# Kernel optimization log

Hardware: AMD Instinct MI355X
Metric: run time of the kernel (lower is better)

The kernel has to match this reference:

```python
import jax, jax.numpy as jnp
import numpy as np

B, L, D = 4, 64, 64
REL_NUM = 16
EMB_NUM = 10000
NEG = -1e9


def gru(x, Wih, Whh, bih, bhh):
    # torch nn.GRU (batch_first), single layer, zero initial state.
    # x: (B,L,Din); Wih: (3H,Din); Whh: (3H,H)
    H = Whh.shape[1]
    gx = x @ Wih.T + bih  # (B,L,3H) precompute input projections

    def step(h, gxt):
        gh = h @ Whh.T + bhh
        xr, xz, xn = jnp.split(gxt, 3, axis=-1)
        hr, hz, hn = jnp.split(gh, 3, axis=-1)
        rg = jax.nn.sigmoid(xr + hr)
        zg = jax.nn.sigmoid(xz + hz)
        ng = jnp.tanh(xn + rg * hn)
        h_new = (1.0 - zg) * ng + zg * h
        return h_new, h_new

    h0 = jnp.zeros((x.shape[0], H), x.dtype)
    _, ys = jax.lax.scan(step, h0, jnp.swapaxes(gx, 0, 1))
    return jnp.swapaxes(ys, 0, 1)  # (B,L,H)


def setup_inputs() -> dict:
    key = jax.random.key(0)
    ks = jax.random.split(key, 20)
    D2 = D // 2
    emb_table = jax.random.normal(ks[0], (EMB_NUM + 1, D), jnp.float32) * 0.1
    emb_table = emb_table.at[0].set(0.0)  # padding_idx=0
    rel_table = jax.random.normal(ks[1], (REL_NUM, D * D), jnp.float32) * 0.05
    rel_table = rel_table.at[0].set(0.0)  # padding_idx=0
    inp = {
        "x": jax.random.randint(ks[2], (B, L), 0, EMB_NUM, jnp.int64) if False else jax.random.randint(ks[2], (B, L), 0, EMB_NUM).astype(jnp.int32),
        "y": jax.random.randint(ks[3], (B,), 0, 2).astype(jnp.int32),
        "r": jax.random.randint(ks[4], (B, L, L), 0, REL_NUM).astype(jnp.int32),
        "l": jax.random.randint(ks[5], (B,), 0, 63).astype(jnp.int32),
        "emb_table": emb_table,
        "rel_table": rel_table,
        "attn_out_W": jax.random.normal(ks[6], (D, D), jnp.float32) * 0.1,
        "attn_out_b": jnp.zeros((D,), jnp.float32),
        "gru_Wih": jax.random.normal(ks[7], (3 * D, D), jnp.float32) * 0.1,
        "gru_Whh": jax.random.normal(ks[8], (3 * D, D), jnp.float32) * 0.1,
        "gru_bih": jax.random.normal(ks[9], (3 * D,), jnp.float32) * 0.01,
        "gru_bhh": jax.random.normal(ks[10], (3 * D,), jnp.float32) * 0.01,
        "out_Wih": jax.random.normal(ks[11], (3, D), jnp.float32) * 0.1,
        "out_Whh": jax.random.normal(ks[12], (3, 1), jnp.float32) * 0.1,
        "out_bih": jax.random.normal(ks[13], (3,), jnp.float32) * 0.01,
        "out_bhh": jax.random.normal(ks[14], (3,), jnp.float32) * 0.01,
        "cls_W1": jax.random.normal(ks[15], (D2, D), jnp.float32) * 0.1,
        "cls_b1": jnp.zeros((D2,), jnp.float32),
        "cls_W2": jax.random.normal(ks[16], (2, D2), jnp.float32) * 0.1,
        "cls_b2": jnp.zeros((2,), jnp.float32),
    }
    return inp


def reference(x, y, r, l, emb_table, rel_table, attn_out_W, attn_out_b,
              gru_Wih, gru_Whh, gru_bih, gru_bhh,
              out_Wih, out_Whh, out_bih, out_bhh,
              cls_W1, cls_b1, cls_W2, cls_b2):
    o = emb_table[x]  # (B,L,D)

    # faithful to torch loop bug: mask[:, :l[i]+1]=1 for all i -> cols < max(l)+1
    mask = jnp.arange(L) < (jnp.max(l) + 1)  # (L,)

    # RelationAttentionBatch: gather per-(i,j) DxD relation matrix, two matvecs
    rel = rel_table[r].reshape(r.shape[0], L, L, D, D)  # (B,L,L,D,D) big gather
    scores = jnp.einsum('bid,bijde,bje->bij', o, rel, o)  # q^T M k
    scores = jnp.where(r > 0, scores, NEG)
    p_attn = jax.nn.softmax(scores, axis=-1)  # dropout off (eval)
    o = jnp.einsum('bij,bjd->bid', p_attn, o) @ attn_out_W.T + attn_out_b

    # GRU layer
    o = gru(o, gru_Wih, gru_Whh, gru_bih, gru_bhh)  # (B,L,D)

    # output GRU -> global attention pooling
    ga = gru(o, out_Wih, out_Whh, out_bih, out_bhh)[..., 0]  # (B,L)
    ga = jnp.where(mask[None, :], ga, NEG)
    ga = jax.nn.softmax(ga, axis=-1)
    c = jnp.einsum('bl,bld->bd', ga, o)  # (B,D)

    # classifier (dropout off)
    h = jax.nn.relu(c @ cls_W1.T + cls_b1)
    logits = h @ cls_W2.T + cls_b2  # (B,2)
    y_hat = jax.nn.softmax(logits, axis=-1)
    logp = jax.nn.log_softmax(logits, axis=-1)
    loss = -jnp.mean(logp[jnp.arange(logits.shape[0]), y])
    return y_hat, loss
```

## Files before the change

### kernel.cpp

```cpp
#include <hip/hip_runtime.h>
#include <math.h>

#define BB 4
#define LL 64
#define DD 64
#define NEG_ -1e9f
#define NBALLAST 480
#define LOG2E 1.44269504088896340736f

typedef _Float16 h2 __attribute__((ext_vector_type(2)));

__device__ __forceinline__ float rcp_(float x) { return __builtin_amdgcn_rcpf(x); }
__device__ __forceinline__ float fast_sigmoid(float x) { return rcp_(1.0f + __expf(-x)); }
__device__ __forceinline__ float fast_tanh(float x) { return fmaf(-2.0f, rcp_(__expf(2.0f * x) + 1.0f), 1.0f); }

__global__ __launch_bounds__(256) void attn_kernel(
    const int* __restrict__ x, const int* __restrict__ r,
    const float* __restrict__ emb, const float* __restrict__ rel,
    const float* __restrict__ aW, const float* __restrict__ ab,
    const float* __restrict__ Wih, const float* __restrict__ bih,
    float* __restrict__ gx, int* __restrict__ done)
{
    const int i = blockIdx.x, b = blockIdx.y;
    const int tt = threadIdx.x, lane = tt & 63, wv = tt >> 6;
    __shared__ float o_lds[LL][DD + 1];
    __shared__ float w_lds[16][DD + 1];
    __shared__ float p_lds[LL];
    __shared__ float pv_part[4][DD];
    __shared__ float ao_lds[DD];
    __shared__ float o2_lds[DD];

    if (i == 0 && b == 0 && tt == 0) *done = 0;

    {
        const int j = tt >> 2, q = tt & 3;
        const int row = x[b * LL + j];
        const float4* src = (const float4*)(emb + row * DD + q * 16);
        const float4 v0 = src[0], v1 = src[1], v2 = src[2], v3 = src[3];
        float* dst = &o_lds[j][q * 16];
        dst[0] = v0.x; dst[1] = v0.y; dst[2] = v0.z; dst[3] = v0.w;
        dst[4] = v1.x; dst[5] = v1.y; dst[6] = v1.z; dst[7] = v1.w;
        dst[8] = v2.x; dst[9] = v2.y; dst[10] = v2.z; dst[11] = v2.w;
        dst[12] = v3.x; dst[13] = v3.y; dst[14] = v3.z; dst[15] = v3.w;
    }
    __syncthreads();

    {
        const int eq = lane & 15, dq = lane >> 4;
#pragma unroll
        for (int kk = 0; kk < 4; kk++) {
            const int k = wv * 4 + kk + 1;
            if (k <= 15) {
                float4 acc = make_float4(0.f, 0.f, 0.f, 0.f);
                const float* relb = rel + k * 4096 + eq * 4;
#pragma unroll
                for (int g2 = 0; g2 < 16; g2++) {
                    const int d = g2 * 4 + dq;
                    const float od = o_lds[i][d];
                    const float4 rv4 = *(const float4*)(relb + d * 64);
                    acc.x = fmaf(od, rv4.x, acc.x);
                    acc.y = fmaf(od, rv4.y, acc.y);
                    acc.z = fmaf(od, rv4.z, acc.z);
                    acc.w = fmaf(od, rv4.w, acc.w);
                }
                acc.x += __shfl_xor(acc.x, 16, 64); acc.y += __shfl_xor(acc.y, 16, 64);
                acc.z += __shfl_xor(acc.z, 16, 64); acc.w += __shfl_xor(acc.w, 16, 64);
                acc.x += __shfl_xor(acc.x, 32, 64); acc.y += __shfl_xor(acc.y, 32, 64);
                acc.z += __shfl_xor(acc.z, 32, 64); acc.w += __shfl_xor(acc.w, 32, 64);
                if (dq == 0) {
                    float* wd = &w_lds[k][eq * 4];
                    wd[0] = acc.x; wd[1] = acc.y; wd[2] = acc.z; wd[3] = acc.w;
                }
            }
        }
    }
    __syncthreads();

    if (wv == 0) {
        const int rv = r[(b * LL + i) * LL + lane];
        float s = NEG_;
        if (rv > 0) {
            float a0 = 0.f, a1 = 0.f;
#pragma unroll
            for (int e = 0; e < DD; e += 2) {
                a0 = fmaf(w_lds[rv][e + 0], o_lds[lane][e + 0], a0);
                a1 = fmaf(w_lds[rv][e + 1], o_lds[lane][e + 1], a1);
            }
            s = a0 + a1;
        }
        float mx = s;
        for (int off = 1; off < 64; off <<= 1) mx = fmaxf(mx, __shfl_xor(mx, off, 64));
        const float ex = __expf(s - mx);
        float sum = ex;
        for (int off = 1; off < 64; off <<= 1) sum += __shfl_xor(sum, off, 64);
        p_lds[lane] = ex * rcp_(sum);
    }
    __syncthreads();

    {
        float acc = 0.f;
#pragma unroll
        for (int j = 0; j < 16; j++) {
            const int jj = wv * 16 + j;
            acc = fmaf(p_lds[jj], o_lds[jj][lane], acc);
        }
        pv_part[wv][lane] = acc;
    }
    __syncthreads();
    if (wv == 0)
        ao_lds[lane] = (pv_part[0][lane] + pv_part[1][lane]) + (pv_part[2][lane] + pv_part[3][lane]);
    __syncthreads();

    {
        const int row = tt >> 2, q = tt & 3;
        float a = 0.f;
        const float4* wr4 = (const float4*)(aW + row * DD + q * 16);
#pragma unroll
        for (int e4 = 0; e4 < 4; e4++) {
            const float4 w4 = wr4[e4];
            const float* av = &ao_lds[q * 16 + e4 * 4];
            a = fmaf(av[0], w4.x, a); a = fmaf(av[1], w4.y, a);
            a = fmaf(av[2], w4.z, a); a = fmaf(av[3], w4.w, a);
        }
        a += __shfl_xor(a, 1, 64);
        a += __shfl_xor(a, 2, 64);
        if (q == 0) o2_lds[row] = a + ab[row];
    }
    __syncthreads();

    if (tt < 192) {
        float a = bih[tt];
        const float4* wg4 = (const float4*)(Wih + tt * DD);
#pragma unroll 4
        for (int e4 = 0; e4 < 16; e4++) {
            const float4 w4 = wg4[e4];
            const float* ov = &o2_lds[e4 * 4];
            a = fmaf(ov[0], w4.x, a); a = fmaf(ov[1], w4.y, a);
            a = fmaf(ov[2], w4.z, a); a = fmaf(ov[3], w4.w, a);
        }
        const float scale = (tt < 128) ? -LOG2E : (2.0f * LOG2E);
        gx[(b * LL + i) * 192 + tt] = a * scale;
    }
}

__global__ __launch_bounds__(128, 1) void gru2_kernel(
    const float* __restrict__ gx, const float* __restrict__ Whh, const float* __restrict__ bhh,
    const float* __restrict__ oWih, const float* __restrict__ oWhh,
    const float* __restrict__ obih, const float* __restrict__ obhh,
    const int* __restrict__ lvec, float* __restrict__ cws, int* __restrict__ done,
    const int* __restrict__ y,
    const float* __restrict__ W1, const float* __restrict__ b1,
    const float* __restrict__ W2, const float* __restrict__ b2,
    float* __restrict__ bsink, float* __restrict__ out)
{
    const int tt = threadIdx.x, t = tt & 63, wv = tt >> 6;

    if (blockIdx.x >= BB) {
        float a0 = tt * 1e-6f, a1 = a0 + 1.f, a2 = a0 + 2.f, a3 = a0 + 3.f;
#pragma unroll 8
        for (int it = 0; it < 2000; it++) {
            a0 = fmaf(a0, 1.0000001f, 1e-7f);
            a1 = fmaf(a1, 1.0000001f, 1e-7f);
            a2 = fmaf(a2, 1.0000001f, 1e-7f);
            a3 = fmaf(a3, 1.0000001f, 1e-7f);
        }
        bsink[(blockIdx.x - BB) * 128 + tt] = (a0 + a1) + (a2 + a3);
        return;
    }

    const int b = blockIdx.x;
    __shared__ float gx_lds[LL][192];
    __shared__ float o3[LL][DD + 1];
    __shared__ int prog;
    __shared__ float c_lds[DD];
    __shared__ float h1s[32];
    __shared__ float lgs[2];

    {
        const float4* src = (const float4*)(gx + b * LL * 192);
        float4* dst = (float4*)&gx_lds[0][0];
#pragma unroll 4
        for (int f = 0; f < 24; f++) dst[f * 128 + tt] = src[f * 128 + tt];
    }
    if (tt == 0) prog = 0;
    __syncthreads();

    if (wv == 0) {
        h2 whr[32], whz[32], whn[32];
        {
            const float4* r0 = (const float4*)(Whh + t * DD);
            const float4* r1 = (const float4*)(Whh + (DD + t) * DD);
            const float4* r2 = (const float4*)(Whh + (2 * DD + t) * DD);
#pragma unroll
            for (int e = 0; e < 16; e++) {
                const float4 a = r0[e], bq = r1[e], c = r2[e];
                whr[2 * e + 0] = (h2){(_Float16)(-LOG2E * a.x), (_Float16)(-LOG2E * a.y)};
                whr[2 * e + 1] = (h2){(_Float16)(-LOG2E * a.z), (_Float16)(-LOG2E * a.w)};
                whz[2 * e + 0] = (h2){(_Float16)(-LOG2E * bq.x), (_Float16)(-LOG2E * bq.y)};
                whz[2 * e + 1] = (h2){(_Float16)(-LOG2E * bq.z), (_Float16)(-LOG2E * bq.w)};
                whn[2 * e + 0] = (h2){(_Float16)(2.f * LOG2E * c.x), (_Float16)(2.f * LOG2E * c.y)};
                whn[2 * e + 1] = (h2){(_Float16)(2.f * LOG2E * c.z), (_Float16)(2.f * LOG2E * c.w)};
            }
        }
#pragma unroll
        for (int i2 = 0; i2 < 32; i2++) {
            asm volatile("" : "+v"(whr[i2]), "+v"(whz[i2]), "+v"(whn[i2]));
        }
        const float br = -LOG2E * bhh[t];
        const float bz = -LOG2E * bhh[DD + t];
        const float bn = 2.f * LOG2E * bhh[2 * DD + t];

        float h = 0.0f;
        int pki = 0;
        float g_r = gx_lds[0][t], g_z = gx_lds[0][DD + t], g_n = gx_lds[0][2 * DD + t];

#pragma unroll 1
        for (int l = 0; l < LL; l++) {
            const int ln = (l + 1) & 63;
            const float pg_r = gx_lds[ln][t];
            const float pg_z = gx_lds[ln][DD + t];
            const float pg_n = gx_lds[ln][2 * DD + t];

            float ra0 = g_r + br, ra1 = 0.f, ra2 = 0.f, ra3 = 0.f;
            float za0 = g_z + bz, za1 = 0.f, za2 = 0.f, za3 = 0.f;
            float na0 = bn,       na1 = 0.f, na2 = 0.f, na3 = 0.f;
#pragma unroll
            for (int j = 0; j < 8; j++) {
                const h2 p0 = __builtin_bit_cast(h2, __builtin_amdgcn_readlane(pki, 8 * j + 0));
                const h2 p1 = __builtin_bit_cast(h2, __builtin_amdgcn_readlane(pki, 8 * j + 2));
                const h2 p2_ = __builtin_bit_cast(h2, __builtin_amdgcn_readlane(pki, 8 * j + 4));
                const h2 p3 = __builtin_bit_cast(h2, __builtin_amdgcn_readlane(pki, 8 * j + 6));
                ra0 = __builtin_amdgcn_fdot2(p0, whr[4 * j + 0], ra0, false);
                ra1 = __builtin_amdgcn_fdot2(p1, whr[4 * j + 1], ra1, false);
                ra2 = __builtin_amdgcn_fdot2(p2_, whr[4 * j + 2], ra2, false);
                ra3 = __builtin_amdgcn_fdot2(p3, whr[4 * j + 3], ra3, false);
                za0 = __builtin_amdgcn_fdot2(p0, whz[4 * j + 0], za0, false);
                za1 = __builtin_amdgcn_fdot2(p1, whz[4 * j + 1], za1, false);
                za2 = __builtin_amdgcn_fdot2(p2_, whz[4 * j + 2], za2, false);
                za3 = __builtin_amdgcn_fdot2(p3, whz[4 * j + 3], za3, false);
                na0 = __builtin_amdgcn_fdot2(p0, whn[4 * j + 0], na0, false);
                na1 = __builtin_amdgcn_fdot2(p1, whn[4 * j + 1], na1, false);
                na2 = __builtin_amdgcn_fdot2(p2_, whn[4 * j + 2], na2, false);
                na3 = __builtin_amdgcn_fdot2(p3, whn[4 * j + 3], na3, false);
            }
            const float yr = (ra0 + ra1) + (ra2 + ra3);
            const float yz = (za0 + za1) + (za2 + za3);
            const float hn = (na0 + na1) + (na2 + na3);

            const float rg = rcp_(1.0f + __builtin_amdgcn_exp2f(yr));
            const float zg = rcp_(1.0f + __builtin_amdgcn_exp2f(yz));
            const float ng = fmaf(-2.0f,
                rcp_(1.0f + __builtin_amdgcn_exp2f(fmaf(rg, hn, g_n))), 1.0f);
            h = fmaf(zg, h - ng, ng);
            o3[l][t] = h;

            if ((l & 3) == 3 && t == 0)
                __hip_atomic_store(&prog, l + 1, __ATOMIC_RELEASE,
                                   __HIP_MEMORY_SCOPE_WORKGROUP);

            const int hxi = __builtin_amdgcn_update_dpp(
                0, __builtin_bit_cast(int, h), 0xB1, 0xF, 0xF, true);
            pki = __builtin_bit_cast(int,
                __builtin_amdgcn_cvt_pkrtz(h, __builtin_bit_cast(float, hxi)));

            g_r = pg_r; g_z = pg_z; g_n = pg_n;
        }
        return;
    }

    const float wm0 = oWih[t], wm1 = oWih[DD + t], wm2 = oWih[2 * DD + t];
    const float ob0 = obih[0], ob1 = obih[1], ob2 = obih[2];
    const float w0 = oWhh[0], w1 = oWhh[1], w2 = oWhh[2];
    const float c0 = obhh[0], c1 = obhh[1], c2 = obhh[2];
    const int maxl = max(max(lvec[0], lvec[1]), max(lvec[2], lvec[3]));

    float hh = 0.0f, pv = 0.0f;
#pragma unroll 1
    for (int l = 0; l < LL; l++) {
        if ((l & 3) == 0) {
            while (__hip_atomic_load(&prog, __ATOMIC_ACQUIRE,
                                     __HIP_MEMORY_SCOPE_WORKGROUP) < l + 1) {}
        }
        const float o = o3[l][t];
        float s0 = o * wm0, s1 = o * wm1, s2 = o * wm2;
#pragma unroll
        for (int off = 1; off < 64; off <<= 1) {
            s0 += __shfl_xor(s0, off, 64);
            s1 += __shfl_xor(s1, off, 64);
            s2 += __shfl_xor(s2, off, 64);
        }
        const float rg = fast_sigmoid(s0 + ob0 + fmaf(hh, w0, c0));
        const float zg = fast_sigmoid(s1 + ob1 + fmaf(hh, w1, c1));
        const float ng = fast_tanh(s2 + ob2 + rg * fmaf(hh, w2, c2));
        hh = (1.0f - zg) * ng + zg * hh;
        pv = (t == l) ? hh : pv;
    }

    {
        const float v = (t <= maxl) ? pv : NEG_;
        float mx = v;
        for (int off = 1; off < 64; off <<= 1) mx = fmaxf(mx, __shfl_xor(mx, off, 64));
        const float ex = __expf(v - mx);
        float sum = ex;
        for (int off = 1; off < 64; off <<= 1) sum += __shfl_xor(sum, off, 64);
        pv = ex * rcp_(sum);
    }

    {
        float acc = 0.f;
#pragma unroll 8
        for (int l = 0; l < LL; l++) {
            const float p = __shfl(pv, l, 64);
            acc = fmaf(p, o3[l][t], acc);
        }
        __hip_atomic_store(&cws[b * DD + t], acc, __ATOMIC_RELAXED,
                           __HIP_MEMORY_SCOPE_AGENT);
    }
    __threadfence();
    unsigned int old = 0;
    if (t == 0)
        old = __hip_atomic_fetch_add((unsigned int*)done, 1u, __ATOMIC_ACQ_REL,
                                     __HIP_MEMORY_SCOPE_AGENT);
    old = __shfl(old, 0, 64);

    if (old == BB - 1) {
        __threadfence();
        float loss = 0.0f;
        for (int bb = 0; bb < BB; bb++) {
            c_lds[t] = __hip_atomic_load(&cws[bb * DD + t], __ATOMIC_RELAXED,
                                         __HIP_MEMORY_SCOPE_AGENT);
            if (t < 32) {
                float a = b1[t];
                const float* wr = W1 + t * DD;
                for (int d = 0; d < DD; d++) a = fmaf(c_lds[d], wr[d], a);
                h1s[t] = fmaxf(a, 0.0f);
            }
            if (t < 2) {
                float a = b2[t];
                const float* wr = W2 + t * 32;
                for (int m2 = 0; m2 < 32; m2++) a = fmaf(h1s[m2], wr[m2], a);
                lgs[t] = a;
            }
            if (t == 0) {
                const float l0 = lgs[0], l1 = lgs[1];
                const float mx = fmaxf(l0, l1);
                const float e0 = __expf(l0 - mx), e1 = __expf(l1 - mx);
                const float s = e0 + e1;
                out[bb * 2 + 0] = e0 / s;
                out[bb * 2 + 1] = e1 / s;
                const float lp = ((y[bb] == 1) ? l1 : l0) - mx - __logf(s);
                loss -= lp * 0.25f;
            }
        }
        if (t == 0) out[8] = loss;
    }
}

extern "C" void kernel_launch(void* const* d_in, const int* in_sizes, int n_in,
                              void* d_out, int out_size, void* d_ws, size_t ws_size,
                              hipStream_t stream)
{
    const int*   x    = (const int*)d_in[0];
    const int*   y    = (const int*)d_in[1];
    const int*   r    = (const int*)d_in[2];
    const int*   l    = (const int*)d_in[3];
    const float* emb  = (const float*)d_in[4];
    const float* rel  = (const float*)d_in[5];
    const float* aW   = (const float*)d_in[6];
    const float* ab   = (const float*)d_in[7];
    const float* Wih  = (const float*)d_in[8];
    const float* Whh  = (const float*)d_in[9];
    const float* bih  = (const float*)d_in[10];
    const float* bhh  = (const float*)d_in[11];
    const float* oWih = (const float*)d_in[12];
    const float* oWhh = (const float*)d_in[13];
    const float* obih = (const float*)d_in[14];
    const float* obhh = (const float*)d_in[15];
    const float* W1   = (const float*)d_in[16];
    const float* b1   = (const float*)d_in[17];
    const float* W2   = (const float*)d_in[18];
    const float* b2   = (const float*)d_in[19];

    float* ws    = (float*)d_ws;
    float* gx    = ws;
    float* cws   = ws + 49152;
    int*   done  = (int*)(ws + 49152 + 256);
    float* bsink = ws + 49152 + 256 + 64;

    attn_kernel<<<dim3(LL, BB), 256, 0, stream>>>(x, r, emb, rel, aW, ab, Wih, bih,
                                                  gx, done);
    gru2_kernel<<<BB + NBALLAST, 128, 0, stream>>>(gx, Whh, bhh, oWih, oWhh, obih,
                                                   obhh, l, cws, done, y, W1, b1,
                                                   W2, b2, bsink, (float*)d_out);
}
```

Before: 46.47 us.

## Fuse attention and GRU kernels into one launch with per-row readiness flags

Merges the attention kernel and the GRU/pooling kernel into a single launch. The extra blocks per batch run the GRU and spin on per-row flags published by the attention blocks, so the recurrence can start on early rows while later rows are still being computed. The GRU now reads gx from global memory one step ahead instead of staging it all in LDS, and the busy-work ballast blocks are removed. The cost is a memset launch to clear the flags, and a deadlock risk if the attention blocks cannot all be resident at once.

```diff
diff --git a/kernel.cpp b/kernel.cpp
--- a/kernel.cpp
+++ b/kernel.cpp
@@ -5,7 +5,6 @@
 #define LL 64
 #define DD 64
 #define NEG_ -1e9f
-#define NBALLAST 480
 #define LOG2E 1.44269504088896340736f
 
 typedef _Float16 h2 __attribute__((ext_vector_type(2)));
@@ -14,178 +13,182 @@
 __device__ __forceinline__ float fast_sigmoid(float x) { return rcp_(1.0f + __expf(-x)); }
 __device__ __forceinline__ float fast_tanh(float x) { return fmaf(-2.0f, rcp_(__expf(2.0f * x) + 1.0f), 1.0f); }
 
-__global__ __launch_bounds__(256) void attn_kernel(
+struct AttnS {
+    float o_lds[LL][DD + 1];
+    float w_lds[16][DD + 1];
+    float p_lds[LL];
+    float pv_part[4][DD];
+    float ao_lds[DD];
+    float o2_lds[DD];
+};
+struct GruS {
+    float o3[LL][DD + 1];
+    float c_lds[DD];
+    float h1s[32];
+    float lgs[2];
+};
+
+__global__ __launch_bounds__(256, 1) void mega_kernel(
     const int* __restrict__ x, const int* __restrict__ r,
     const float* __restrict__ emb, const float* __restrict__ rel,
     const float* __restrict__ aW, const float* __restrict__ ab,
     const float* __restrict__ Wih, const float* __restrict__ bih,
-    float* __restrict__ gx, int* __restrict__ done)
-{
-    const int i = blockIdx.x, b = blockIdx.y;
-    const int tt = threadIdx.x, lane = tt & 63, wv = tt >> 6;
-    __shared__ float o_lds[LL][DD + 1];
-    __shared__ float w_lds[16][DD + 1];
-    __shared__ float p_lds[LL];
-    __shared__ float pv_part[4][DD];
-    __shared__ float ao_lds[DD];
-    __shared__ float o2_lds[DD];
-
-    if (i == 0 && b == 0 && tt == 0) *done = 0;
-
-    {
-        const int j = tt >> 2, q = tt & 3;
-        const int row = x[b * LL + j];
-        const float4* src = (const float4*)(emb + row * DD + q * 16);
-        const float4 v0 = src[0], v1 = src[1], v2 = src[2], v3 = src[3];
-        float* dst = &o_lds[j][q * 16];
-        dst[0] = v0.x; dst[1] = v0.y; dst[2] = v0.z; dst[3] = v0.w;
-        dst[4] = v1.x; dst[5] = v1.y; dst[6] = v1.z; dst[7] = v1.w;
-        dst[8] = v2.x; dst[9] = v2.y; dst[10] = v2.z; dst[11] = v2.w;
-        dst[12] = v3.x; dst[13] = v3.y; dst[14] = v3.z; dst[15] = v3.w;
-    }
-    __syncthreads();
-
-    {
-        const int eq = lane & 15, dq = lane >> 4;
-#pragma unroll
-        for (int kk = 0; kk < 4; kk++) {
-            const int k = wv * 4 + kk + 1;
-            if (k <= 15) {
-                float4 acc = make_float4(0.f, 0.f, 0.f, 0.f);
-                const float* relb = rel + k * 4096 + eq * 4;
-#pragma unroll
-                for (int g2 = 0; g2 < 16; g2++) {
-                    const int d = g2 * 4 + dq;
-                    const float od = o_lds[i][d];
-                    const float4 rv4 = *(const float4*)(relb + d * 64);
-                    acc.x = fmaf(od, rv4.x, acc.x);
-                    acc.y = fmaf(od, rv4.y, acc.y);
-                    acc.z = fmaf(od, rv4.z, acc.z);
-                    acc.w = fmaf(od, rv4.w, acc.w);
-                }
-                acc.x += __shfl_xor(acc.x, 16, 64); acc.y += __shfl_xor(acc.y, 16, 64);
-                acc.z += __shfl_xor(acc.z, 16, 64); acc.w += __shfl_xor(acc.w, 16, 64);
-                acc.x += __shfl_xor(acc.x, 32, 64); acc.y += __shfl_xor(acc.y, 32, 64);
-                acc.z += __shfl_xor(acc.z, 32, 64); acc.w += __shfl_xor(acc.w, 32, 64);
-                if (dq == 0) {
-                    float* wd = &w_lds[k][eq * 4];
-                    wd[0] = acc.x; wd[1] = acc.y; wd[2] = acc.z; wd[3] = acc.w;
-                }
-            }
-        }
-    }
-    __syncthreads();
-
-    if (wv == 0) {
-        const int rv = r[(b * LL + i) * LL + lane];
-        float s = NEG_;
-        if (rv > 0) {
-            float a0 = 0.f, a1 = 0.f;
-#pragma unroll
-            for (int e = 0; e < DD; e += 2) {
-                a0 = fmaf(w_lds[rv][e + 0], o_lds[lane][e + 0], a0);
-                a1 = fmaf(w_lds[rv][e + 1], o_lds[lane][e + 1], a1);
-            }
-            s = a0 + a1;
-        }
-        float mx = s;
-        for (int off = 1; off < 64; off <<= 1) mx = fmaxf(mx, __shfl_xor(mx, off, 64));
-        const float ex = __expf(s - mx);
-        float sum = ex;
-        for (int off = 1; off < 64; off <<= 1) sum += __shfl_xor(sum, off, 64);
-        p_lds[lane] = ex * rcp_(sum);
-    }
-    __syncthreads();
-
-    {
-        float acc = 0.f;
-#pragma unroll
-        for (int j = 0; j < 16; j++) {
-            const int jj = wv * 16 + j;
-            acc = fmaf(p_lds[jj], o_lds[jj][lane], acc);
-        }
-        pv_part[wv][lane] = acc;
-    }
-    __syncthreads();
-    if (wv == 0)
-        ao_lds[lane] = (pv_part[0][lane] + pv_part[1][lane]) + (pv_part[2][lane] + pv_part[3][lane]);
-    __syncthreads();
-
-    {
-        const int row = tt >> 2, q = tt & 3;
-        float a = 0.f;
-        const float4* wr4 = (const float4*)(aW + row * DD + q * 16);
-#pragma unroll
-        for (int e4 = 0; e4 < 4; e4++) {
-            const float4 w4 = wr4[e4];
-            const float* av = &ao_lds[q * 16 + e4 * 4];
-            a = fmaf(av[0], w4.x, a); a = fmaf(av[1], w4.y, a);
-            a = fmaf(av[2], w4.z, a); a = fmaf(av[3], w4.w, a);
-        }
-        a += __shfl_xor(a, 1, 64);
-        a += __shfl_xor(a, 2, 64);
-        if (q == 0) o2_lds[row] = a + ab[row];
-    }
-    __syncthreads();
-
-    if (tt < 192) {
-        float a = bih[tt];
-        const float4* wg4 = (const float4*)(Wih + tt * DD);
-#pragma unroll 4
-        for (int e4 = 0; e4 < 16; e4++) {
-            const float4 w4 = wg4[e4];
-            const float* ov = &o2_lds[e4 * 4];
-            a = fmaf(ov[0], w4.x, a); a = fmaf(ov[1], w4.y, a);
-            a = fmaf(ov[2], w4.z, a); a = fmaf(ov[3], w4.w, a);
-        }
-        const float scale = (tt < 128) ? -LOG2E : (2.0f * LOG2E);
-        gx[(b * LL + i) * 192 + tt] = a * scale;
-    }
-}
-
-__global__ __launch_bounds__(128, 1) void gru2_kernel(
-    const float* __restrict__ gx, const float* __restrict__ Whh, const float* __restrict__ bhh,
+    const float* __restrict__ Whh, const float* __restrict__ bhh,
     const float* __restrict__ oWih, const float* __restrict__ oWhh,
     const float* __restrict__ obih, const float* __restrict__ obhh,
-    const int* __restrict__ lvec, float* __restrict__ cws, int* __restrict__ done,
-    const int* __restrict__ y,
+    const int* __restrict__ lvec, const int* __restrict__ y,
     const float* __restrict__ W1, const float* __restrict__ b1,
     const float* __restrict__ W2, const float* __restrict__ b2,
-    float* __restrict__ bsink, float* __restrict__ out)
+    float* __restrict__ gx, float* __restrict__ cws,
+    int* __restrict__ flags, int* __restrict__ done,
+    float* __restrict__ out)
 {
-    const int tt = threadIdx.x, t = tt & 63, wv = tt >> 6;
-
-    if (blockIdx.x >= BB) {
-        float a0 = tt * 1e-6f, a1 = a0 + 1.f, a2 = a0 + 2.f, a3 = a0 + 3.f;
-#pragma unroll 8
-        for (int it = 0; it < 2000; it++) {
-            a0 = fmaf(a0, 1.0000001f, 1e-7f);
-            a1 = fmaf(a1, 1.0000001f, 1e-7f);
-            a2 = fmaf(a2, 1.0000001f, 1e-7f);
-            a3 = fmaf(a3, 1.0000001f, 1e-7f);
-        }
-        bsink[(blockIdx.x - BB) * 128 + tt] = (a0 + a1) + (a2 + a3);
+    const int bx = blockIdx.x, b = blockIdx.y;
+    const int tt = threadIdx.x, lane = tt & 63, wv = tt >> 6;
+    __shared__ union { AttnS a; GruS g; } sm;
+    __shared__ int wm_sm;
+    __shared__ int prog;
+
+    if (bx < LL) {
+        const int i = bx;
+        {
+            const int j = tt >> 2, q = tt & 3;
+            const int row = x[b * LL + j];
+            const float4* src = (const float4*)(emb + row * DD + q * 16);
+            const float4 v0 = src[0], v1 = src[1], v2 = src[2], v3 = src[3];
+            float* dst = &sm.a.o_lds[j][q * 16];
+            dst[0] = v0.x; dst[1] = v0.y; dst[2] = v0.z; dst[3] = v0.w;
+            dst[4] = v1.x; dst[5] = v1.y; dst[6] = v1.z; dst[7] = v1.w;
+            dst[8] = v2.x; dst[9] = v2.y; dst[10] = v2.z; dst[11] = v2.w;
+            dst[12] = v3.x; dst[13] = v3.y; dst[14] = v3.z; dst[15] = v3.w;
+        }
+        __syncthreads();
+
+        {
+            const int eq = lane & 15, dq = lane >> 4;
+#pragma unroll
+            for (int kk = 0; kk < 4; kk++) {
+                const int k = wv * 4 + kk + 1;
+                if (k <= 15) {
+                    float4 acc = make_float4(0.f, 0.f, 0.f, 0.f);
+                    const float* relb = rel + k * 4096 + eq * 4;
+#pragma unroll
+                    for (int g2 = 0; g2 < 16; g2++) {
+                        const int d = g2 * 4 + dq;
+                        const float od = sm.a.o_lds[i][d];
+                        const float4 rv4 = *(const float4*)(relb + d * 64);
+                        acc.x = fmaf(od, rv4.x, acc.x);
+                        acc.y = fmaf(od, rv4.y, acc.y);
+                        acc.z = fmaf(od, rv4.z, acc.z);
+                        acc.w = fmaf(od, rv4.w, acc.w);
+                    }
+                    acc.x += __shfl_xor(acc.x, 16, 64); acc.y += __shfl_xor(acc.y, 16, 64);
+                    acc.z += __shfl_xor(acc.z, 16, 64); acc.w += __shfl_xor(acc.w, 16, 64);
+                    acc.x += __shfl_xor(acc.x, 32, 64); acc.y += __shfl_xor(acc.y, 32, 64);
+                    acc.z += __shfl_xor(acc.z, 32, 64); acc.w += __shfl_xor(acc.w, 32, 64);
+                    if (dq == 0) {
+                        float* wd = &sm.a.w_lds[k][eq * 4];
+                        wd[0] = acc.x; wd[1] = acc.y; wd[2] = acc.z; wd[3] = acc.w;
+                    }
+                }
+            }
+        }
+        __syncthreads();
+
+        if (wv == 0) {
+            const int rv = r[(b * LL + i) * LL + lane];
+            float s = NEG_;
+            if (rv > 0) {
+                float a0 = 0.f, a1 = 0.f;
+#pragma unroll
+                for (int e = 0; e < DD; e += 2) {
+                    a0 = fmaf(sm.a.w_lds[rv][e + 0], sm.a.o_lds[lane][e + 0], a0);
+                    a1 = fmaf(sm.a.w_lds[rv][e + 1], sm.a.o_lds[lane][e + 1], a1);
+                }
+                s = a0 + a1;
+            }
+            float mx = s;
+            for (int off = 1; off < 64; off <<= 1) mx = fmaxf(mx, __shfl_xor(mx, off, 64));
+            const float ex = __expf(s - mx);
+            float sum = ex;
+            for (int off = 1; off < 64; off <<= 1) sum += __shfl_xor(sum, off, 64);
+            sm.a.p_lds[lane] = ex * rcp_(sum);
+        }
+        __syncthreads();
+
+        {
+            float acc = 0.f;
+#pragma unroll
+            for (int j = 0; j < 16; j++) {
+                const int jj = wv * 16 + j;
+                acc = fmaf(sm.a.p_lds[jj], sm.a.o_lds[jj][lane], acc);
+            }
+            sm.a.pv_part[wv][lane] = acc;
+        }
+        __syncthreads();
+        if (wv == 0)
+            sm.a.ao_lds[lane] = (sm.a.pv_part[0][lane] + sm.a.pv_part[1][lane]) +
+                                (sm.a.pv_part[2][lane] + sm.a.pv_part[3][lane]);
+        __syncthreads();
+
+        {
+            const int row = tt >> 2, q = tt & 3;
+            float a = 0.f;
+            const float4* wr4 = (const float4*)(aW + row * DD + q * 16);
+#pragma unroll
+            for (int e4 = 0; e4 < 4; e4++) {
+                const float4 w4 = wr4[e4];
+                const float* av = &sm.a.ao_lds[q * 16 + e4 * 4];
+                a = fmaf(av[0], w4.x, a); a = fmaf(av[1], w4.y, a);
+                a = fmaf(av[2], w4.z, a); a = fmaf(av[3], w4.w, a);
+            }
+            a += __shfl_xor(a, 1, 64);
+            a += __shfl_xor(a, 2, 64);
+            if (q == 0) sm.a.o2_lds[row] = a + ab[row];
+        }
+        __syncthreads();
+
+        if (tt < 192) {
+            float a = bih[tt];
+            const float4* wg4 = (const float4*)(Wih + tt * DD);
+#pragma unroll 4
+            for (int e4 = 0; e4 < 16; e4++) {
+                const float4 w4 = wg4[e4];
+                const float* ov = &sm.a.o2_lds[e4 * 4];
+                a = fmaf(ov[0], w4.x, a); a = fmaf(ov[1], w4.y, a);
+                a = fmaf(ov[2], w4.z, a); a = fmaf(ov[3], w4.w, a);
+            }
+            const float scale = (tt < 128) ? -LOG2E : (2.0f * LOG2E);
+            gx[(b * LL + i) * 192 + tt] = a * scale;
+        }
+        __syncthreads();
+        if (tt == 0) {
+            __threadfence();
+            __hip_atomic_store(&flags[b * LL + i], 1, __ATOMIC_RELEASE,
+                               __HIP_MEMORY_SCOPE_AGENT);
+        }
         return;
     }
 
-    const int b = blockIdx.x;
-    __shared__ float gx_lds[LL][192];
-    __shared__ float o3[LL][DD + 1];
-    __shared__ int prog;
-    __shared__ float c_lds[DD];
-    __shared__ float h1s[32];
-    __shared__ float lgs[2];
-
-    {
-        const float4* src = (const float4*)(gx + b * LL * 192);
-        float4* dst = (float4*)&gx_lds[0][0];
-#pragma unroll 4
-        for (int f = 0; f < 24; f++) dst[f * 128 + tt] = src[f * 128 + tt];
-    }
-    if (tt == 0) prog = 0;
+    if (tt == 0) { wm_sm = 0; prog = 0; }
     __syncthreads();
 
+    if (wv == 2) {
+        for (int w = 0; w < 8; w++) {
+            for (;;) {
+                const int f = __hip_atomic_load(&flags[b * LL + 8 * w + (lane & 7)],
+                                                __ATOMIC_ACQUIRE, __HIP_MEMORY_SCOPE_AGENT);
+                if (__all(f != 0)) break;
+            }
+            if (lane == 0)
+                __hip_atomic_store(&wm_sm, w + 1, __ATOMIC_RELEASE,
+                                   __HIP_MEMORY_SCOPE_WORKGROUP);
+        }
+        return;
+    }
+
     if (wv == 0) {
+        const int t = lane;
         h2 whr[32], whz[32], whn[32];
         {
             const float4* r0 = (const float4*)(Whh + t * DD);
@@ -210,16 +213,22 @@
         const float bz = -LOG2E * bhh[DD + t];
         const float bn = 2.f * LOG2E * bhh[2 * DD + t];
 
+        while (__hip_atomic_load(&wm_sm, __ATOMIC_ACQUIRE,
+                                 __HIP_MEMORY_SCOPE_WORKGROUP) < 1) {}
+        const float* gxb = gx + b * LL * 192;
+        float g_r = gxb[t], g_z = gxb[DD + t], g_n = gxb[2 * DD + t];
+
         float h = 0.0f;
         int pki = 0;
-        float g_r = gx_lds[0][t], g_z = gx_lds[0][DD + t], g_n = gx_lds[0][2 * DD + t];
-
 #pragma unroll 1
         for (int l = 0; l < LL; l++) {
             const int ln = (l + 1) & 63;
-            const float pg_r = gx_lds[ln][t];
-            const float pg_z = gx_lds[ln][DD + t];
-            const float pg_n = gx_lds[ln][2 * DD + t];
+            if ((ln & 7) == 0 && ln != 0) {
+                while (__hip_atomic_load(&wm_sm, __ATOMIC_ACQUIRE,
+                                         __HIP_MEMORY_SCOPE_WORKGROUP) <= (ln >> 3)) {}
+            }
+            const float* rp = gxb + ln * 192;
+            const float pg_r = rp[t], pg_z = rp[DD + t], pg_n = rp[2 * DD + t];
 
             float ra0 = g_r + br, ra1 = 0.f, ra2 = 0.f, ra3 = 0.f;
             float za0 = g_z + bz, za1 = 0.f, za2 = 0.f, za3 = 0.f;
@@ -252,7 +261,7 @@
             const float ng = fmaf(-2.0f,
                 rcp_(1.0f + __builtin_amdgcn_exp2f(fmaf(rg, hn, g_n))), 1.0f);
             h = fmaf(zg, h - ng, ng);
-            o3[l][t] = h;
+            sm.g.o3[l][t] = h;
 
             if ((l & 3) == 3 && t == 0)
                 __hip_atomic_store(&prog, l + 1, __ATOMIC_RELEASE,
@@ -268,6 +277,9 @@
         return;
     }
 
+    if (wv != 1) return;
+
+    const int t = lane;
     const float wm0 = oWih[t], wm1 = oWih[DD + t], wm2 = oWih[2 * DD + t];
     const float ob0 = obih[0], ob1 = obih[1], ob2 = obih[2];
     const float w0 = oWhh[0], w1 = oWhh[1], w2 = oWhh[2];
@@ -281,7 +293,7 @@
             while (__hip_atomic_load(&prog, __ATOMIC_ACQUIRE,
                                      __HIP_MEMORY_SCOPE_WORKGROUP) < l + 1) {}
         }
-        const float o = o3[l][t];
+        const float o = sm.g.o3[l][t];
         float s0 = o * wm0, s1 = o * wm1, s2 = o * wm2;
 #pragma unroll
         for (int off = 1; off < 64; off <<= 1) {
@@ -311,7 +323,7 @@
 #pragma unroll 8
         for (int l = 0; l < LL; l++) {
             const float p = __shfl(pv, l, 64);
-            acc = fmaf(p, o3[l][t], acc);
+            acc = fmaf(p, sm.g.o3[l][t], acc);
         }
         __hip_atomic_store(&cws[b * DD + t], acc, __ATOMIC_RELAXED,
                            __HIP_MEMORY_SCOPE_AGENT);
@@ -327,22 +339,22 @@
         __threadfence();
         float loss = 0.0f;
         for (int bb = 0; bb < BB; bb++) {
-            c_lds[t] = __hip_atomic_load(&cws[bb * DD + t], __ATOMIC_RELAXED,
-                                         __HIP_MEMORY_SCOPE_AGENT);
+            sm.g.c_lds[t] = __hip_atomic_load(&cws[bb * DD + t], __ATOMIC_RELAXED,
+                                              __HIP_MEMORY_SCOPE_AGENT);
             if (t < 32) {
                 float a = b1[t];
                 const float* wr = W1 + t * DD;
-                for (int d = 0; d < DD; d++) a = fmaf(c_lds[d], wr[d], a);
-                h1s[t] = fmaxf(a, 0.0f);
+                for (int d = 0; d < DD; d++) a = fmaf(sm.g.c_lds[d], wr[d], a);
+                sm.g.h1s[t] = fmaxf(a, 0.0f);
             }
             if (t < 2) {
                 float a = b2[t];
                 const float* wr = W2 + t * 32;
-                for (int m2 = 0; m2 < 32; m2++) a = fmaf(h1s[m2], wr[m2], a);
-                lgs[t] = a;
+                for (int m2 = 0; m2 < 32; m2++) a = fmaf(sm.g.h1s[m2], wr[m2], a);
+                sm.g.lgs[t] = a;
             }
             if (t == 0) {
-                const float l0 = lgs[0], l1 = lgs[1];
+                const float l0 = sm.g.lgs[0], l1 = sm.g.lgs[1];
                 const float mx = fmaxf(l0, l1);
                 const float e0 = __expf(l0 - mx), e1 = __expf(l1 - mx);
                 const float s = e0 + e1;
@@ -384,12 +396,11 @@
     float* ws    = (float*)d_ws;
     float* gx    = ws;
     float* cws   = ws + 49152;
-    int*   done  = (int*)(ws + 49152 + 256);
-    float* bsink = ws + 49152 + 256 + 64;
-
-    attn_kernel<<<dim3(LL, BB), 256, 0, stream>>>(x, r, emb, rel, aW, ab, Wih, bih,
-                                                  gx, done);
-    gru2_kernel<<<BB + NBALLAST, 128, 0, stream>>>(gx, Whh, bhh, oWih, oWhh, obih,
-                                                   obhh, l, cws, done, y, W1, b1,
-                                                   W2, b2, bsink, (float*)d_out);
+    int*   flags = (int*)(ws + 49152 + 256);
+    int*   done  = flags + 256;
+
+    hipMemsetAsync(flags, 0, (256 + 1) * sizeof(int), stream);
+    mega_kernel<<<dim3(LL + 1, BB), 256, 0, stream>>>(
+        x, r, emb, rel, aW, ab, Wih, bih, Whh, bhh, oWih, oWhh, obih, obhh,
+        l, y, W1, b1, W2, b2, gx, cws, flags, done, (float*)d_out);
 }
```

Measured after the change: 61.33 us. +32.0%, slower.
